# Kernel tuning notes

Hardware: AMD Instinct MI355X
Metric: run time of the kernel (lower is better)

## Reference

```python
import jax, jax.numpy as jnp
import numpy as np

B, Hh, Ww, C = 64, 24, 24, 768
HID = 576
MAX_LEN = 1024
W_SCALE = 0.02  # small init so exp(k) stays numerically tame


def setup_inputs() -> dict:
    key = jax.random.key(0)
    ks = jax.random.split(key, 8)
    x = jax.random.normal(ks[0], (B, Hh, Ww, C), dtype=jnp.float32)
    Wq = jax.random.normal(ks[1], (C, HID), dtype=jnp.float32) * W_SCALE
    Wk = jax.random.normal(ks[2], (C, HID), dtype=jnp.float32) * W_SCALE
    Wv = jax.random.normal(ks[3], (C, HID), dtype=jnp.float32) * W_SCALE
    Wo = jax.random.normal(ks[4], (HID, C), dtype=jnp.float32) * W_SCALE
    bq = jnp.zeros((HID,), jnp.float32)
    bk = jnp.zeros((HID,), jnp.float32)
    bv = jnp.zeros((HID,), jnp.float32)
    bo = jnp.zeros((C,), jnp.float32)
    u = jax.random.normal(ks[5], (MAX_LEN, HID), dtype=jnp.float32) * 0.01
    vp = jax.random.normal(ks[6], (MAX_LEN, HID), dtype=jnp.float32) * 0.01
    return {"x": x, "Wq": Wq, "bq": bq, "Wk": Wk, "bk": bk, "Wv": Wv,
            "bv": bv, "Wo": Wo, "bo": bo, "u": u, "vp": vp}


def reference(x, Wq, bq, Wk, bk, Wv, bv, Wo, bo, u, vp):
    b, h, w, c = x.shape
    t = h * w  # sequence length after flatten
    xf = x.reshape(b, t, c)                      # [B,T,C]
    q = xf @ Wq + bq                             # [B,T,HID]
    k = xf @ Wk + bk
    v = xf @ Wv + bv
    wmat = u.T @ vp                              # [HID,HID] pairwise position bias
    w_bias = wmat[:t, :t][None]                  # [1,T,T]
    # faithful to torch: max over dim 0 (batch for k; trivial singleton for w_bias)
    max_k = jnp.max(k, axis=0, keepdims=True)    # [1,T,HID]
    max_wb = jnp.max(w_bias, axis=0, keepdims=True)
    exp_k = jnp.exp(k - max_k)                   # [B,T,HID]
    exp_wb = jnp.exp(w_bias - max_wb)            # [1,T,T]
    num = jnp.matmul(exp_wb, exp_k * v)          # [B,T,HID]
    den = jnp.matmul(exp_wb, exp_k)              # [B,T,HID]
    y = jax.nn.sigmoid(q) * num / den            # [B,T,HID]
    out = y @ Wo + bo                            # [B,T,C]
    return out.reshape(b, h, w, c)
```

## Files before the change

kernel.cpp:

```cpp
#include <hip/hip_runtime.h>
#include <hip/hip_bf16.h>
#include <stdint.h>


typedef __bf16 vbf16x8 __attribute__((ext_vector_type(8)));
typedef float  vf32x4  __attribute__((ext_vector_type(4)));

#define BB   64
#define TT   576
#define CC   768
#define HID  576
#define NQKV 1792
#define KPAD 640
#define MR   (BB*TT)

__device__ __forceinline__ unsigned short f2bf(float f) {
    union { float f; unsigned u; } v; v.f = f;
    unsigned r = v.u + 0x7fffu + ((v.u >> 16) & 1u);
    return (unsigned short)(r >> 16);
}
__device__ __forceinline__ float bf2f(unsigned short b) {
    union { unsigned u; float f; } v; v.u = ((unsigned)b) << 16;
    return v.f;
}

__global__ void prep_kernel(const float* __restrict__ Wq, const float* __restrict__ Wk,
                            const float* __restrict__ Wv, const float* __restrict__ Wo,
                            const float* __restrict__ bq, const float* __restrict__ bk,
                            const float* __restrict__ bv,
                            unsigned short* __restrict__ WqkvT,
                            unsigned short* __restrict__ WoT,
                            float* __restrict__ bqkv)
{
    int idx = blockIdx.x * 256 + threadIdx.x;
    const int NW1 = NQKV * CC;
    const int NW2 = CC * KPAD;
    if (idx < NW1) {
        int n = idx / CC, k = idx % CC;
        float v = 0.f;
        if      (n < 576)  v = Wq[k * HID + n];
        else if (n < 1152) v = Wk[k * HID + (n - 576)];
        else if (n < 1728) v = Wv[k * HID + (n - 1152)];
        WqkvT[idx] = f2bf(v);
    } else if (idx < NW1 + NW2) {
        int i = idx - NW1;
        int c = i / KPAD, h = i % KPAD;
        WoT[i] = (h < HID) ? f2bf(Wo[h * CC + c]) : (unsigned short)0;
    } else if (idx < NW1 + NW2 + NQKV) {
        int n = idx - NW1 - NW2;
        float v = 0.f;
        if      (n < 576)  v = bq[n];
        else if (n < 1152) v = bk[n - 576];
        else if (n < 1728) v = bv[n - 1152];
        bqkv[n] = v;
    }
}

__global__ void convx_kernel(const float* __restrict__ x, unsigned short* __restrict__ xb, int n4)
{
    int i = blockIdx.x * 256 + threadIdx.x;
    if (i >= n4) return;
    float4 a = ((const float4*)x)[i];
    uint2 o;
    o.x = (unsigned)f2bf(a.x) | ((unsigned)f2bf(a.y) << 16);
    o.y = (unsigned)f2bf(a.z) | ((unsigned)f2bf(a.w) << 16);
    ((uint2*)xb)[i] = o;
}


#define BARR() asm volatile("s_barrier" ::: "memory")
#define MFMA_BEGIN() do { asm volatile("s_waitcnt lgkmcnt(0)" ::: "memory"); \
                          __builtin_amdgcn_sched_barrier(0); \
                          __builtin_amdgcn_s_setprio(1); } while (0)
#define MFMA_END() do { __builtin_amdgcn_s_setprio(0); \
                        __builtin_amdgcn_sched_barrier(0); } while (0)
#define VMCNT2() asm volatile("s_waitcnt vmcnt(2)" ::: "memory")
#define VMCNT0() asm volatile("s_waitcnt vmcnt(0)" ::: "memory")

#define STG(BI, MAT, H, KT, G) do { \
    const unsigned short* _s0 = (G) + (size_t)(H) * 128 * ldk + (size_t)(KT) * 64 + off0; \
    const unsigned short* _s1 = (G) + (size_t)(H) * 128 * ldk + (size_t)(KT) * 64 + off1; \
    __builtin_amdgcn_global_load_lds((const __attribute__((address_space(1))) void*)_s0, \
        (__attribute__((address_space(3))) void*)&lds[BI][MAT][(H) * 8192 + wave * 512], 16, 0, 0); \
    __builtin_amdgcn_global_load_lds((const __attribute__((address_space(1))) void*)_s1, \
        (__attribute__((address_space(3))) void*)&lds[BI][MAT][(H) * 8192 + 4096 + wave * 512], 16, 0, 0); \
} while (0)

__device__ __forceinline__ void read_a4(const char* L, int base, int fr, int kg, vbf16x8 o[4][2]) {
#pragma unroll
    for (int m = 0; m < 4; ++m)
#pragma unroll
        for (int ks = 0; ks < 2; ++ks) {
            int R = base + m * 16 + fr;
            o[m][ks] = *(const vbf16x8*)(L + (size_t)R * 128 + ((((ks * 4 + kg) ^ (R & 7))) << 4));
        }
}
__device__ __forceinline__ void read_b2(const char* L, int base, int fr, int kg, vbf16x8 o[2][2]) {
#pragma unroll
    for (int n = 0; n < 2; ++n)
#pragma unroll
        for (int ks = 0; ks < 2; ++ks) {
            int R = base + n * 16 + fr;
            o[n][ks] = *(const vbf16x8*)(L + (size_t)R * 128 + ((((ks * 4 + kg) ^ (R & 7))) << 4));
        }
}
__device__ __forceinline__ void mfma16(vf32x4 acc[8][4], const vbf16x8 a[4][2],
                                       const vbf16x8 b[2][2], int mo, int no) {
#pragma unroll
    for (int m = 0; m < 4; ++m)
#pragma unroll
        for (int n = 0; n < 2; ++n)
#pragma unroll
            for (int ks = 0; ks < 2; ++ks)
                acc[mo + m][no + n] = __builtin_amdgcn_mfma_f32_16x16x32_bf16(
                    a[m][ks], b[n][ks], acc[mo + m][no + n], 0, 0, 0);
}

template <int EPI>
__global__ __launch_bounds__(512, 2) void gemm8p(const unsigned short* __restrict__ A,
                                                 const unsigned short* __restrict__ Bt,
                                                 void* __restrict__ Cv,
                                                 const float* __restrict__ bias,
                                                 int N, int ldk, int NITER, int nbn)
{
    __shared__ unsigned short lds[2][2][16384];
    int tid = threadIdx.x;
    int lane = tid & 63, wave = tid >> 6;
    int fr = lane & 15, kg = lane >> 4;
    int wm = wave >> 2, wn = wave & 3;

    int cpx = gridDim.x >> 3;
    int wg = (blockIdx.x & 7) * cpx + (blockIdx.x >> 3);
    int bm = wg / nbn, bn = wg % nbn;

    const unsigned short* Ag = A + (size_t)bm * 256 * ldk;
    const unsigned short* Bg = Bt + (size_t)bn * 256 * ldk;

    int c0 = tid, c1 = 512 + tid;
    int r0 = c0 >> 3, q0 = c0 & 7, r1 = c1 >> 3, q1 = c1 & 7;
    size_t off0 = (size_t)r0 * ldk + (size_t)((q0 ^ (r0 & 7)) << 3);
    size_t off1 = (size_t)r1 * ldk + (size_t)((q1 ^ (r1 & 7)) << 3);

    vf32x4 acc[8][4] = {};
    vbf16x8 a0[4][2], a1[4][2], b0[2][2], b1[2][2];

    STG(0, 0, 0, 0, Ag); STG(0, 0, 1, 0, Ag);
    STG(0, 1, 0, 0, Bg); STG(0, 1, 1, 0, Bg);
    STG(1, 0, 0, 1, Ag);
    VMCNT2();
    BARR();

    for (int t = 0; t < NITER; ++t) {
        bool last = (t == NITER - 1);
        int k1 = 2 * t + 1, k2 = 2 * t + 2, k3 = 2 * t + 3;
        {
            const char* LA = (const char*)lds[0][0];
            const char* LB = (const char*)lds[0][1];
            read_a4(LA, wm * 128, fr, kg, a0);
            read_b2(LB, wn * 64, fr, kg, b0);
            STG(1, 0, 1, k1, Ag);
            MFMA_BEGIN(); mfma16(acc, a0, b0, 0, 0); MFMA_END(); BARR();
            read_b2(LB, wn * 64 + 32, fr, kg, b1);
            STG(1, 1, 0, k1, Bg);
            MFMA_BEGIN(); mfma16(acc, a0, b1, 0, 2); MFMA_END(); BARR();
            read_a4(LA, wm * 128 + 64, fr, kg, a1);
            STG(1, 1, 1, k1, Bg);
            MFMA_BEGIN(); mfma16(acc, a1, b1, 4, 2); MFMA_END(); BARR();
            if (!last) STG(0, 0, 0, k2, Ag);
            MFMA_BEGIN(); mfma16(acc, a1, b0, 4, 0); MFMA_END();
            if (!last) VMCNT2(); else VMCNT0();
            BARR();
        }
        {
            const char* LA = (const char*)lds[1][0];
            const char* LB = (const char*)lds[1][1];
            read_a4(LA, wm * 128, fr, kg, a0);
            read_b2(LB, wn * 64, fr, kg, b0);
            if (!last) STG(0, 0, 1, k2, Ag);
            MFMA_BEGIN(); mfma16(acc, a0, b0, 0, 0); MFMA_END(); BARR();
            read_b2(LB, wn * 64 + 32, fr, kg, b1);
            if (!last) STG(0, 1, 0, k2, Bg);
            MFMA_BEGIN(); mfma16(acc, a0, b1, 0, 2); MFMA_END(); BARR();
            read_a4(LA, wm * 128 + 64, fr, kg, a1);
            if (!last) STG(0, 1, 1, k2, Bg);
            MFMA_BEGIN(); mfma16(acc, a1, b1, 4, 2); MFMA_END(); BARR();
            if (!last) STG(1, 0, 0, k3, Ag);
            MFMA_BEGIN(); mfma16(acc, a1, b0, 4, 0); MFMA_END();
            if (!last) VMCNT2(); else VMCNT0();
            BARR();
        }
    }

    int row0 = bm * 256 + wm * 128 + kg * 4;
    int col0 = bn * 256 + wn * 64;
#pragma unroll
    for (int m = 0; m < 8; ++m) {
#pragma unroll
        for (int n = 0; n < 4; ++n) {
            int c = col0 + n * 16 + fr;
            float bb = bias[c];
            int r = row0 + m * 16;
#pragma unroll
            for (int j = 0; j < 4; ++j) {
                float v = acc[m][n][j] + bb;
                if (EPI == 0) ((unsigned short*)Cv)[(size_t)(r + j) * N + c] = f2bf(v);
                else          ((float*)Cv)[(size_t)(r + j) * N + c] = v;
            }
        }
    }
}

__global__ void maxk_kernel(const unsigned short* __restrict__ qkv, float* __restrict__ maxk)
{
    int idx = blockIdx.x * 256 + threadIdx.x;
    if (idx >= TT * HID) return;
    int t = idx / HID, h = idx % HID;
    const unsigned short* p = qkv + (size_t)t * NQKV + 576 + h;
    const size_t stride = (size_t)TT * NQKV;
    float m0 = -1e30f, m1 = -1e30f, m2 = -1e30f, m3 = -1e30f;
#pragma unroll 4
    for (int b = 0; b < BB; b += 4) {
        m0 = fmaxf(m0, bf2f(p[(size_t)(b + 0) * stride]));
        m1 = fmaxf(m1, bf2f(p[(size_t)(b + 1) * stride]));
        m2 = fmaxf(m2, bf2f(p[(size_t)(b + 2) * stride]));
        m3 = fmaxf(m3, bf2f(p[(size_t)(b + 3) * stride]));
    }
    maxk[idx] = fmaxf(fmaxf(m0, m1), fmaxf(m2, m3));
}

__global__ void numden_kernel(const unsigned short* __restrict__ qkv,
                              const float* __restrict__ maxk,
                              float* __restrict__ num_p, float* __restrict__ den_p)
{
    int b = blockIdx.x, tc = blockIdx.y, h = threadIdx.x;
    float num = 0.f, den = 0.f;
    int t0 = tc * 144;
    for (int t = t0; t < t0 + 144; ++t) {
        const unsigned short* row = qkv + (size_t)(b * TT + t) * NQKV;
        float kk = bf2f(row[576 + h]);
        float vv = bf2f(row[1152 + h]);
        float e  = __expf(kk - maxk[t * HID + h]);
        den += e;
        num += e * vv;
    }
    int o = (tc * BB + b) * HID + h;
    num_p[o] = num;
    den_p[o] = den;
}

__global__ void y_kernel(const unsigned short* __restrict__ qkv,
                         const float* __restrict__ num_p, const float* __restrict__ den_p,
                         unsigned short* __restrict__ y)
{
    int idx = blockIdx.x * 256 + threadIdx.x;
    if (idx >= MR * (KPAD / 8)) return;
    int h8 = idx % (KPAD / 8), row = idx / (KPAD / 8);
    if (h8 >= HID / 8) {
        uint4 z = {0, 0, 0, 0};
        *(uint4*)(y + (size_t)row * KPAD + h8 * 8) = z;
        return;
    }
    int b = row / TT;
    uint4 q4 = *(const uint4*)(qkv + (size_t)row * NQKV + h8 * 8);
    float num[8], den[8];
#pragma unroll
    for (int j = 0; j < 8; ++j) { num[j] = 0.f; den[j] = 0.f; }
#pragma unroll
    for (int tc = 0; tc < 4; ++tc) {
        const float* np = num_p + (size_t)(tc * BB + b) * HID + h8 * 8;
        const float* dp = den_p + (size_t)(tc * BB + b) * HID + h8 * 8;
#pragma unroll
        for (int j = 0; j < 8; ++j) { num[j] += np[j]; den[j] += dp[j]; }
    }
    unsigned qs[4] = { q4.x, q4.y, q4.z, q4.w };
    unsigned o[4];
#pragma unroll
    for (int w2 = 0; w2 < 4; ++w2) {
        float qa = bf2f((unsigned short)(qs[w2] & 0xffff));
        float qb = bf2f((unsigned short)(qs[w2] >> 16));
        float r0 = num[w2 * 2]     / den[w2 * 2];
        float r1 = num[w2 * 2 + 1] / den[w2 * 2 + 1];
        float y0 = (1.f / (1.f + __expf(-qa))) * r0;
        float y1 = (1.f / (1.f + __expf(-qb))) * r1;
        o[w2] = (unsigned)f2bf(y0) | ((unsigned)f2bf(y1) << 16);
    }
    uint4 ov; ov.x = o[0]; ov.y = o[1]; ov.z = o[2]; ov.w = o[3];
    *(uint4*)(y + (size_t)row * KPAD + h8 * 8) = ov;
}

extern "C" void kernel_launch(void* const* d_in, const int* in_sizes, int n_in,
                              void* d_out, int out_size, void* d_ws, size_t ws_size,
                              hipStream_t stream)
{
    const float* x  = (const float*)d_in[0];
    const float* Wq = (const float*)d_in[1];
    const float* bq = (const float*)d_in[2];
    const float* Wk = (const float*)d_in[3];
    const float* bk = (const float*)d_in[4];
    const float* Wv = (const float*)d_in[5];
    const float* bv = (const float*)d_in[6];
    const float* Wo = (const float*)d_in[7];
    const float* bo = (const float*)d_in[8];
    float* out = (float*)d_out;

    char* ws = (char*)d_ws;
    size_t off = 0;
    auto alloc = [&](size_t bytes) -> void* {
        off = (off + 255) & ~(size_t)255;
        void* p = ws + off;
        off += bytes;
        return p;
    };

    unsigned short* xb    = (unsigned short*)alloc((size_t)MR * CC * 2);
    unsigned short* WqkvT = (unsigned short*)alloc((size_t)NQKV * CC * 2);
    unsigned short* WoT   = (unsigned short*)alloc((size_t)CC * KPAD * 2);
    float*          bqkv  = (float*)alloc((size_t)NQKV * 4);
    unsigned short* qkv   = (unsigned short*)alloc((size_t)MR * NQKV * 2);
    float*          maxk  = (float*)alloc((size_t)TT * HID * 4);
    float*          num_p = (float*)alloc((size_t)4 * BB * HID * 4);
    float*          den_p = (float*)alloc((size_t)4 * BB * HID * 4);
    unsigned short* yb    = xb;

    {
        int total = NQKV * CC + CC * KPAD + NQKV;
        prep_kernel<<<dim3((total + 255) / 256), dim3(256), 0, stream>>>(
            Wq, Wk, Wv, Wo, bq, bk, bv, WqkvT, WoT, bqkv);
    }
    {
        int n4 = MR * CC / 4;
        convx_kernel<<<dim3(n4 / 256), dim3(256), 0, stream>>>(x, xb, n4);
    }
    gemm8p<0><<<dim3((MR / 256) * (NQKV / 256)), dim3(512), 0, stream>>>(
        xb, WqkvT, (void*)qkv, bqkv, NQKV, CC, CC / 128, NQKV / 256);
    maxk_kernel<<<dim3(TT * HID / 256), dim3(256), 0, stream>>>(qkv, maxk);
    numden_kernel<<<dim3(BB, 4), dim3(HID), 0, stream>>>(qkv, maxk, num_p, den_p);
    {
        int total = MR * (KPAD / 8);
        y_kernel<<<dim3(total / 256), dim3(256), 0, stream>>>(qkv, num_p, den_p, yb);
    }
    gemm8p<1><<<dim3((MR / 256) * (CC / 256)), dim3(512), 0, stream>>>(
        yb, WoT, (void*)out, bo, CC, KPAD, KPAD / 128, CC / 256);
}
```

Baseline: 261.6 us.

## Drop K padding in output GEMM and pack QKV buffer to its real width

The GEMM now counts K in 64-wide tiles and handles an odd tile count with a tail step. This lets the output projection run with K=576 instead of a zero-padded 640, which saves one K tile of loads and MFMAs per block and removes the padding writes in y_kernel. The QKV intermediate is stored with a 1728 stride instead of 1792, and the padded columns are skipped in the epilogue, which cuts write and read traffic. The prefetch order changes so B is loaded before A, with a different vmcnt budget. That schedule change could alter load/compute overlap or introduce races if the wait counts are wrong.

```diff
diff --git a/kernel.cpp b/kernel.cpp
--- a/kernel.cpp
+++ b/kernel.cpp
@@ -10,8 +10,8 @@
 #define TT   576
 #define CC   768
 #define HID  576
-#define NQKV 1792
-#define KPAD 640
+#define LQ   1728
+#define NBQ  1792
 #define MR   (BB*TT)
 
 __device__ __forceinline__ unsigned short f2bf(float f) {
@@ -33,8 +33,8 @@
                             float* __restrict__ bqkv)
 {
     int idx = blockIdx.x * 256 + threadIdx.x;
-    const int NW1 = NQKV * CC;
-    const int NW2 = CC * KPAD;
+    const int NW1 = NBQ * CC;
+    const int NW2 = CC * HID;
     if (idx < NW1) {
         int n = idx / CC, k = idx % CC;
         float v = 0.f;
@@ -44,9 +44,9 @@
         WqkvT[idx] = f2bf(v);
     } else if (idx < NW1 + NW2) {
         int i = idx - NW1;
-        int c = i / KPAD, h = i % KPAD;
-        WoT[i] = (h < HID) ? f2bf(Wo[h * CC + c]) : (unsigned short)0;
-    } else if (idx < NW1 + NW2 + NQKV) {
+        int c = i / HID, h = i % HID;
+        WoT[i] = f2bf(Wo[h * CC + c]);
+    } else if (idx < NW1 + NW2 + NBQ) {
         int n = idx - NW1 - NW2;
         float v = 0.f;
         if      (n < 576)  v = bq[n];
@@ -74,7 +74,7 @@
                           __builtin_amdgcn_s_setprio(1); } while (0)
 #define MFMA_END() do { __builtin_amdgcn_s_setprio(0); \
                         __builtin_amdgcn_sched_barrier(0); } while (0)
-#define VMCNT2() asm volatile("s_waitcnt vmcnt(2)" ::: "memory")
+#define VMCNT4() asm volatile("s_waitcnt vmcnt(4)" ::: "memory")
 #define VMCNT0() asm volatile("s_waitcnt vmcnt(0)" ::: "memory")
 
 #define STG(BI, MAT, H, KT, G) do { \
@@ -121,7 +121,8 @@
                                                  const unsigned short* __restrict__ Bt,
                                                  void* __restrict__ Cv,
                                                  const float* __restrict__ bias,
-                                                 int N, int ldk, int NITER, int nbn)
+                                                 int ldc, int Nstore,
+                                                 int ldk, int NT, int nbn)
 {
     __shared__ unsigned short lds[2][2][16384];
     int tid = threadIdx.x;
@@ -144,31 +145,32 @@
     vf32x4 acc[8][4] = {};
     vbf16x8 a0[4][2], a1[4][2], b0[2][2], b1[2][2];
 
+    STG(0, 1, 0, 0, Bg); STG(0, 1, 1, 0, Bg);
     STG(0, 0, 0, 0, Ag); STG(0, 0, 1, 0, Ag);
-    STG(0, 1, 0, 0, Bg); STG(0, 1, 1, 0, Bg);
-    STG(1, 0, 0, 1, Ag);
-    VMCNT2();
+    STG(1, 1, 0, 1, Bg); STG(1, 1, 1, 1, Bg);
+    VMCNT4();
     BARR();
 
-    for (int t = 0; t < NITER; ++t) {
-        bool last = (t == NITER - 1);
+    int NH = NT >> 1;
+    for (int t = 0; t < NH; ++t) {
         int k1 = 2 * t + 1, k2 = 2 * t + 2, k3 = 2 * t + 3;
+        bool s2 = (k2 < NT), s3 = (k3 < NT);
         {
             const char* LA = (const char*)lds[0][0];
             const char* LB = (const char*)lds[0][1];
             read_a4(LA, wm * 128, fr, kg, a0);
             read_b2(LB, wn * 64, fr, kg, b0);
-            STG(1, 0, 1, k1, Ag);
+            STG(1, 0, 0, k1, Ag);
             MFMA_BEGIN(); mfma16(acc, a0, b0, 0, 0); MFMA_END(); BARR();
             read_b2(LB, wn * 64 + 32, fr, kg, b1);
-            STG(1, 1, 0, k1, Bg);
+            STG(1, 0, 1, k1, Ag);
             MFMA_BEGIN(); mfma16(acc, a0, b1, 0, 2); MFMA_END(); BARR();
             read_a4(LA, wm * 128 + 64, fr, kg, a1);
-            STG(1, 1, 1, k1, Bg);
+            if (s2) STG(0, 1, 0, k2, Bg);
             MFMA_BEGIN(); mfma16(acc, a1, b1, 4, 2); MFMA_END(); BARR();
-            if (!last) STG(0, 0, 0, k2, Ag);
+            if (s2) STG(0, 1, 1, k2, Bg);
             MFMA_BEGIN(); mfma16(acc, a1, b0, 4, 0); MFMA_END();
-            if (!last) VMCNT2(); else VMCNT0();
+            if (s2) VMCNT4(); else VMCNT0();
             BARR();
         }
         {
@@ -176,19 +178,33 @@
             const char* LB = (const char*)lds[1][1];
             read_a4(LA, wm * 128, fr, kg, a0);
             read_b2(LB, wn * 64, fr, kg, b0);
-            if (!last) STG(0, 0, 1, k2, Ag);
+            if (s2) STG(0, 0, 0, k2, Ag);
             MFMA_BEGIN(); mfma16(acc, a0, b0, 0, 0); MFMA_END(); BARR();
             read_b2(LB, wn * 64 + 32, fr, kg, b1);
-            if (!last) STG(0, 1, 0, k2, Bg);
+            if (s2) STG(0, 0, 1, k2, Ag);
             MFMA_BEGIN(); mfma16(acc, a0, b1, 0, 2); MFMA_END(); BARR();
             read_a4(LA, wm * 128 + 64, fr, kg, a1);
-            if (!last) STG(0, 1, 1, k2, Bg);
+            if (s3) STG(1, 1, 0, k3, Bg);
             MFMA_BEGIN(); mfma16(acc, a1, b1, 4, 2); MFMA_END(); BARR();
-            if (!last) STG(1, 0, 0, k3, Ag);
+            if (s3) STG(1, 1, 1, k3, Bg);
             MFMA_BEGIN(); mfma16(acc, a1, b0, 4, 0); MFMA_END();
-            if (!last) VMCNT2(); else VMCNT0();
+            VMCNT4();
             BARR();
         }
+    }
+    if (NT & 1) {
+        VMCNT0();
+        BARR();
+        const char* LA = (const char*)lds[0][0];
+        const char* LB = (const char*)lds[0][1];
+        read_a4(LA, wm * 128, fr, kg, a0);
+        read_b2(LB, wn * 64, fr, kg, b0);
+        read_b2(LB, wn * 64 + 32, fr, kg, b1);
+        read_a4(LA, wm * 128 + 64, fr, kg, a1);
+        MFMA_BEGIN();
+        mfma16(acc, a0, b0, 0, 0); mfma16(acc, a0, b1, 0, 2);
+        mfma16(acc, a1, b1, 4, 2); mfma16(acc, a1, b0, 4, 0);
+        MFMA_END();
     }
 
     int row0 = bm * 256 + wm * 128 + kg * 4;
@@ -198,13 +214,15 @@
 #pragma unroll
         for (int n = 0; n < 4; ++n) {
             int c = col0 + n * 16 + fr;
-            float bb = bias[c];
-            int r = row0 + m * 16;
-#pragma unroll
-            for (int j = 0; j < 4; ++j) {
-                float v = acc[m][n][j] + bb;
-                if (EPI == 0) ((unsigned short*)Cv)[(size_t)(r + j) * N + c] = f2bf(v);
-                else          ((float*)Cv)[(size_t)(r + j) * N + c] = v;
+            if (c < Nstore) {
+                float bb = bias[c];
+                int r = row0 + m * 16;
+#pragma unroll
+                for (int j = 0; j < 4; ++j) {
+                    float v = acc[m][n][j] + bb;
+                    if (EPI == 0) ((unsigned short*)Cv)[(size_t)(r + j) * ldc + c] = f2bf(v);
+                    else          ((float*)Cv)[(size_t)(r + j) * ldc + c] = v;
+                }
             }
         }
     }
@@ -215,8 +233,8 @@
     int idx = blockIdx.x * 256 + threadIdx.x;
     if (idx >= TT * HID) return;
     int t = idx / HID, h = idx % HID;
-    const unsigned short* p = qkv + (size_t)t * NQKV + 576 + h;
-    const size_t stride = (size_t)TT * NQKV;
+    const unsigned short* p = qkv + (size_t)t * LQ + 576 + h;
+    const size_t stride = (size_t)TT * LQ;
     float m0 = -1e30f, m1 = -1e30f, m2 = -1e30f, m3 = -1e30f;
 #pragma unroll 4
     for (int b = 0; b < BB; b += 4) {
@@ -236,7 +254,7 @@
     float num = 0.f, den = 0.f;
     int t0 = tc * 144;
     for (int t = t0; t < t0 + 144; ++t) {
-        const unsigned short* row = qkv + (size_t)(b * TT + t) * NQKV;
+        const unsigned short* row = qkv + (size_t)(b * TT + t) * LQ;
         float kk = bf2f(row[576 + h]);
         float vv = bf2f(row[1152 + h]);
         float e  = __expf(kk - maxk[t * HID + h]);
@@ -253,15 +271,10 @@
                          unsigned short* __restrict__ y)
 {
     int idx = blockIdx.x * 256 + threadIdx.x;
-    if (idx >= MR * (KPAD / 8)) return;
-    int h8 = idx % (KPAD / 8), row = idx / (KPAD / 8);
-    if (h8 >= HID / 8) {
-        uint4 z = {0, 0, 0, 0};
-        *(uint4*)(y + (size_t)row * KPAD + h8 * 8) = z;
-        return;
-    }
+    if (idx >= MR * (HID / 8)) return;
+    int h8 = idx % (HID / 8), row = idx / (HID / 8);
     int b = row / TT;
-    uint4 q4 = *(const uint4*)(qkv + (size_t)row * NQKV + h8 * 8);
+    uint4 q4 = *(const uint4*)(qkv + (size_t)row * LQ + h8 * 8);
     float num[8], den[8];
 #pragma unroll
     for (int j = 0; j < 8; ++j) { num[j] = 0.f; den[j] = 0.f; }
@@ -285,7 +298,7 @@
         o[w2] = (unsigned)f2bf(y0) | ((unsigned)f2bf(y1) << 16);
     }
     uint4 ov; ov.x = o[0]; ov.y = o[1]; ov.z = o[2]; ov.w = o[3];
-    *(uint4*)(y + (size_t)row * KPAD + h8 * 8) = ov;
+    *(uint4*)(y + (size_t)row * HID + h8 * 8) = ov;
 }
 
 extern "C" void kernel_launch(void* const* d_in, const int* in_sizes, int n_in,
@@ -313,17 +326,17 @@
     };
 
     unsigned short* xb    = (unsigned short*)alloc((size_t)MR * CC * 2);
-    unsigned short* WqkvT = (unsigned short*)alloc((size_t)NQKV * CC * 2);
-    unsigned short* WoT   = (unsigned short*)alloc((size_t)CC * KPAD * 2);
-    float*          bqkv  = (float*)alloc((size_t)NQKV * 4);
-    unsigned short* qkv   = (unsigned short*)alloc((size_t)MR * NQKV * 2);
+    unsigned short* WqkvT = (unsigned short*)alloc((size_t)NBQ * CC * 2);
+    unsigned short* WoT   = (unsigned short*)alloc((size_t)CC * HID * 2);
+    float*          bqkv  = (float*)alloc((size_t)NBQ * 4);
+    unsigned short* qkv   = (unsigned short*)alloc((size_t)MR * LQ * 2);
     float*          maxk  = (float*)alloc((size_t)TT * HID * 4);
     float*          num_p = (float*)alloc((size_t)4 * BB * HID * 4);
     float*          den_p = (float*)alloc((size_t)4 * BB * HID * 4);
     unsigned short* yb    = xb;
 
     {
-        int total = NQKV * CC + CC * KPAD + NQKV;
+        int total = NBQ * CC + CC * HID + NBQ;
         prep_kernel<<<dim3((total + 255) / 256), dim3(256), 0, stream>>>(
             Wq, Wk, Wv, Wo, bq, bk, bv, WqkvT, WoT, bqkv);
     }
@@ -331,14 +344,14 @@
         int n4 = MR * CC / 4;
         convx_kernel<<<dim3(n4 / 256), dim3(256), 0, stream>>>(x, xb, n4);
     }
-    gemm8p<0><<<dim3((MR / 256) * (NQKV / 256)), dim3(512), 0, stream>>>(
-        xb, WqkvT, (void*)qkv, bqkv, NQKV, CC, CC / 128, NQKV / 256);
+    gemm8p<0><<<dim3((MR / 256) * (NBQ / 256)), dim3(512), 0, stream>>>(
+        xb, WqkvT, (void*)qkv, bqkv, LQ, LQ, CC, CC / 64, NBQ / 256);
     maxk_kernel<<<dim3(TT * HID / 256), dim3(256), 0, stream>>>(qkv, maxk);
     numden_kernel<<<dim3(BB, 4), dim3(HID), 0, stream>>>(qkv, maxk, num_p, den_p);
     {
-        int total = MR * (KPAD / 8);
+        int total = MR * (HID / 8);
         y_kernel<<<dim3(total / 256), dim3(256), 0, stream>>>(qkv, num_p, den_p, yb);
     }
     gemm8p<1><<<dim3((MR / 256) * (CC / 256)), dim3(512), 0, stream>>>(
-        yb, WoT, (void*)out, bo, CC, KPAD, KPAD / 128, CC / 256);
-}
+        yb, WoT, (void*)out, bo, CC, CC, HID, HID / 64, CC / 256);
+}
```

Measured after the change: 387.9 us. 48.3% more time.
